# Optimization experiments

Hardware: AMD Instinct MI355X
Metric: run time of the kernel (lower is better)

Reference implementation:

```python
import jax, jax.numpy as jnp
import numpy as np

K_H, K_W = 3, 3
STRIDE, PAD = 1, 1
GN_GROUPS = 32
EPS = 1e-5


def setup_inputs() -> dict:
    key = jax.random.key(0)
    k1, k2, k3 = jax.random.split(key, 3)
    B, C, H, W = 4, 256, 64, 64
    Cout = 256
    x = jax.random.normal(k1, (B, C, H, W), jnp.float32)
    offset = jax.random.normal(k2, (B, 2 * K_H * K_W, H, W), jnp.float32)
    weight = jax.random.normal(k3, (Cout, C, K_H, K_W), jnp.float32) * 0.02
    gamma = jnp.ones((Cout,), jnp.float32)
    beta = jnp.zeros((Cout,), jnp.float32)
    return {"x": x, "offset": offset, "weight": weight, "gamma": gamma, "beta": beta}


def _deform_conv(x, offset, weight):
    B, C, H, W = x.shape
    Cout = weight.shape[0]
    K = K_H * K_W
    Ho = (H + 2 * PAD - K_H) // STRIDE + 1
    Wo = (W + 2 * PAD - K_W) // STRIDE + 1
    ky, kx = jnp.meshgrid(jnp.arange(K_H), jnp.arange(K_W), indexing='ij')
    ky = ky.reshape(K).astype(x.dtype)
    kx = kx.reshape(K).astype(x.dtype)
    # base sampling positions per kernel tap
    py_base = (jnp.arange(Ho) * STRIDE - PAD).astype(x.dtype)[None, :] + ky[:, None]  # [K,Ho]
    px_base = (jnp.arange(Wo) * STRIDE - PAD).astype(x.dtype)[None, :] + kx[:, None]  # [K,Wo]
    off = offset.reshape(B, K, 2, Ho, Wo)  # mmcv layout: (dy, dx) pairs per tap
    py = py_base[None, :, :, None] + off[:, :, 0]  # [B,K,Ho,Wo]
    px = px_base[None, :, None, :] + off[:, :, 1]  # [B,K,Ho,Wo]
    y0 = jnp.floor(py)
    x0 = jnp.floor(px)
    ly = py - y0
    lx = px - x0
    xf = x.reshape(B, C, H * W)

    def gather(yi, xi):
        valid = (yi >= 0) & (yi <= H - 1) & (xi >= 0) & (xi <= W - 1)
        yc = jnp.clip(yi, 0, H - 1).astype(jnp.int32)
        xc = jnp.clip(xi, 0, W - 1).astype(jnp.int32)
        idx = yc * W + xc  # [B,K,Ho,Wo]
        vals = jax.vmap(lambda xb, ib: xb[:, ib])(xf, idx)  # [B,C,K,Ho,Wo]
        return vals * valid[:, None].astype(x.dtype)

    g00 = gather(y0, x0)
    g01 = gather(y0, x0 + 1)
    g10 = gather(y0 + 1, x0)
    g11 = gather(y0 + 1, x0 + 1)
    wy = ly[:, None]  # [B,1,K,Ho,Wo]
    wx = lx[:, None]
    val = ((1 - wy) * (1 - wx) * g00 + (1 - wy) * wx * g01
           + wy * (1 - wx) * g10 + wy * wx * g11)  # [B,C,K,Ho,Wo]
    return jnp.einsum('bckhw,ock->bohw', val, weight.reshape(Cout, C, K))


def reference(x, offset, weight, gamma, beta):
    y = _deform_conv(x, offset, weight)  # [B,Cout,Ho,Wo]
    B, C, H, W = y.shape
    yg = y.reshape(B, GN_GROUPS, C // GN_GROUPS, H, W)
    mean = jnp.mean(yg, axis=(2, 3, 4), keepdims=True)
    var = jnp.var(yg, axis=(2, 3, 4), keepdims=True)
    yn = ((yg - mean) * jax.lax.rsqrt(var + EPS)).reshape(B, C, H, W)
    out = yn * gamma[None, :, None, None] + beta[None, :, None, None]
    return jax.nn.relu(out)
```

## Files before the change

kernel.cpp:

```cpp
#include <hip/hip_runtime.h>

typedef unsigned short ushort_t;
typedef __bf16 bf16x8 __attribute__((ext_vector_type(8)));
typedef float f32x4 __attribute__((ext_vector_type(4)));
typedef void __attribute__((address_space(1))) gvoid_t;
typedef void __attribute__((address_space(3))) lvoid_t;

__device__ __forceinline__ float bflo(unsigned u) { return __builtin_bit_cast(float, u << 16); }
__device__ __forceinline__ float bfhi(unsigned u) { return __builtin_bit_cast(float, u & 0xffff0000u); }
__device__ __forceinline__ unsigned f2bf_bits(float f) {
  unsigned u = __builtin_bit_cast(unsigned, f);
  return (u + 0x7fffu + ((u >> 16) & 1u)) >> 16;
}
__device__ __forceinline__ ushort_t f2bf(float f) { return (ushort_t)f2bf_bits(f); }

#define VMWAIT(N) asm volatile("s_waitcnt vmcnt(" #N ")" ::: "memory")
#define LGKM0 asm volatile("s_waitcnt lgkmcnt(0)" ::: "memory")

__global__ __launch_bounds__(256) void k_prep_w(const float* __restrict__ w,
                                                ushort_t* __restrict__ wb) {
  const int idx = blockIdx.x * 256 + threadIdx.x;
  const float* src = w + (size_t)idx * 9;
  #pragma unroll
  for (int k = 0; k < 9; ++k)
    wb[(k << 16) + idx] = f2bf(src[k]);
}

__global__ __launch_bounds__(256) void k_prep_x(const float* __restrict__ x,
                                                ushort_t* __restrict__ xt) {
  __shared__ ushort_t tile[64][68];
  const int bid = blockIdx.x;
  const int b = bid >> 8;
  const int ct = (bid >> 6) & 3;
  const int pt = bid & 63;
  const int t = threadIdx.x;
  const float* xb = x + ((size_t)(b * 256 + ct * 64)) * 4096 + pt * 64;
  #pragma unroll
  for (int i = 0; i < 16; ++i) {
    const int idx = t + 256 * i;
    const int c_l = idx >> 6, p_l = idx & 63;
    tile[c_l][p_l] = f2bf(xb[(size_t)c_l * 4096 + p_l]);
  }
  __syncthreads();
  ushort_t* xo = xt + ((size_t)(b * 4096 + pt * 64)) * 256 + ct * 64;
  #pragma unroll
  for (int i = 0; i < 16; ++i) {
    const int idx = t + 256 * i;
    const int p_l = idx >> 6, c_l = idx & 63;
    xo[(size_t)p_l * 256 + c_l] = tile[c_l][p_l];
  }
}

struct SMeta {
  float w00, w01, w10, w11;
  int i00, i01, i10, i11;
};
__device__ __forceinline__ SMeta meta_for(int h, int gw, int k, float oy, float ox) {
  SMeta m;
  const float py = (float)(h - 1 + k / 3) + oy;
  const float px = (float)(gw - 1 + k % 3) + ox;
  const float fy = floorf(py), fx = floorf(px);
  const float ly = py - fy, lx = px - fx;
  const int iy0 = (int)fy, ix0 = (int)fx;
  const float vy0 = (iy0 >= 0 && iy0 < 64) ? 1.f : 0.f;
  const float vy1 = (iy0 >= -1 && iy0 < 63) ? 1.f : 0.f;
  const float vx0 = (ix0 >= 0 && ix0 < 64) ? 1.f : 0.f;
  const float vx1 = (ix0 >= -1 && ix0 < 63) ? 1.f : 0.f;
  m.w00 = (1.f - ly) * (1.f - lx) * vy0 * vx0;
  m.w01 = (1.f - ly) * lx * vy0 * vx1;
  m.w10 = ly * (1.f - lx) * vy1 * vx0;
  m.w11 = ly * lx * vy1 * vx1;
  const int cy0 = min(max(iy0, 0), 63), cy1 = min(max(iy0 + 1, 0), 63);
  const int cx0 = min(max(ix0, 0), 63), cx1 = min(max(ix0 + 1, 0), 63);
  m.i00 = (cy0 * 64 + cx0) * 256;
  m.i01 = (cy0 * 64 + cx1) * 256;
  m.i10 = (cy1 * 64 + cx0) * 256;
  m.i11 = (cy1 * 64 + cx1) * 256;
  return m;
}

__device__ __forceinline__ unsigned lerp_pack(unsigned a, unsigned b, unsigned c, unsigned d,
                                              float w00, float w01, float w10, float w11) {
  float lo = w00 * bflo(a) + w01 * bflo(b) + w10 * bflo(c) + w11 * bflo(d);
  float hi = w00 * bfhi(a) + w01 * bfhi(b) + w10 * bfhi(c) + w11 * bfhi(d);
  return f2bf_bits(lo) | (f2bf_bits(hi) << 16);
}

__global__ __launch_bounds__(512) void k_gemm(const float* __restrict__ off,
                                              const ushort_t* __restrict__ xt,
                                              const ushort_t* __restrict__ wb,
                                              float* __restrict__ y,
                                              float* __restrict__ stats) {
  __shared__ __attribute__((aligned(16))) ushort_t Abuf[2][64 * 64];
  __shared__ __attribute__((aligned(16))) ushort_t Bbuf[3][256 * 64];

  const int bid = blockIdx.x;
  const int lb = ((bid & 7) << 5) | (bid >> 3);
  const int b = lb >> 6;
  const int h = lb & 63;
  const int t = threadIdx.x;
  const int wave = t >> 6;
  const int lane = t & 63;
  const int wq = lane >> 4;
  const int wr = lane & 15;
  const int wm = wave >> 2;
  const int wn = wave & 3;

  const int s_w = t >> 3;
  const int c8 = t & 7;

  const f32x4 zero = {0.f, 0.f, 0.f, 0.f};
  f32x4 acc[2][4];
  #pragma unroll
  for (int i = 0; i < 2; ++i)
    #pragma unroll
    for (int j = 0; j < 4; ++j) acc[i][j] = zero;

  const ushort_t* xtb = xt + (size_t)b * 4096 * 256;

  float oy[9], ox[9];
  {
    const float* offb = off + (size_t)b * 18 * 4096 + h * 64 + s_w;
    #pragma unroll
    for (int k = 0; k < 9; ++k) {
      oy[k] = offb[(2 * k) * 4096];
      ox[k] = offb[(2 * k + 1) * 4096];
    }
  }

#define GATHER_ISSUE(TAP, C0)                             \
  {                                                       \
    m = meta_for(h, s_w, (TAP), oy[(TAP)], ox[(TAP)]);    \
    const int cc = (C0) + c8 * 8;                         \
    q00 = *(const uint4*)(xtb + m.i00 + cc);              \
    q01 = *(const uint4*)(xtb + m.i01 + cc);              \
    q10 = *(const uint4*)(xtb + m.i10 + cc);              \
    q11 = *(const uint4*)(xtb + m.i11 + cc);              \
  }

#define B_ISSUE(TAP, C0, BUF)                                                                \
  {                                                                                          \
    _Pragma("unroll") for (int i_ = 0; i_ < 4; ++i_) {                                       \
      const int idx_ = i_ * 512 + t;                                                         \
      const int row_ = idx_ >> 3, slot_ = idx_ & 7;                                          \
      const ushort_t* g_ = wb + ((TAP) << 16) + row_ * 256 + (C0) + ((slot_ ^ (row_ & 7)) << 3); \
      __builtin_amdgcn_global_load_lds((gvoid_t*)g_,                                         \
                                       (lvoid_t*)((char*)&Bbuf[(BUF)][0] + idx_ * 16), 16,   \
                                       0, 0);                                                \
    }                                                                                        \
  }

#define A_WRITE(BUF)                                                         \
  {                                                                          \
    uint4 r;                                                                 \
    r.x = lerp_pack(q00.x, q01.x, q10.x, q11.x, m.w00, m.w01, m.w10, m.w11); \
    r.y = lerp_pack(q00.y, q01.y, q10.y, q11.y, m.w00, m.w01, m.w10, m.w11); \
    r.z = lerp_pack(q00.z, q01.z, q10.z, q11.z, m.w00, m.w01, m.w10, m.w11); \
    r.w = lerp_pack(q00.w, q01.w, q10.w, q11.w, m.w00, m.w01, m.w10, m.w11); \
    *(uint4*)&Abuf[(BUF)][s_w * 64 + ((c8 ^ (s_w & 7)) << 3)] = r;           \
  }

  {
    uint4 q00, q01, q10, q11;
    SMeta m;
    GATHER_ISSUE(0, 0);
    B_ISSUE(0, 0, 0);
    B_ISSUE(0, 64, 1);
    VMWAIT(8);
    A_WRITE(0);
    LGKM0;
    __builtin_amdgcn_s_barrier();
  }

  #pragma unroll
  for (int n = 0; n < 36; ++n) {
    const int curB = n % 3;
    const int curA = n & 1;
    uint4 q00, q01, q10, q11;
    SMeta m;
    if (n < 35) {
      GATHER_ISSUE((n + 1) >> 2, ((n + 1) & 3) << 6);
    }
    if (n < 34) {
      B_ISSUE((n + 2) >> 2, ((n + 2) & 3) << 6, (n + 2) % 3);
    }
    VMWAIT(12);
    #pragma unroll
    for (int ks = 0; ks < 2; ++ks) {
      bf16x8 af[2], bfr[4];
      #pragma unroll
      for (int tm = 0; tm < 2; ++tm) {
        const int row = wm * 32 + tm * 16 + wr;
        const int slot = (ks * 4 + wq) ^ (row & 7);
        af[tm] = *(const bf16x8*)&Abuf[curA][row * 64 + slot * 8];
      }
      #pragma unroll
      for (int tn = 0; tn < 4; ++tn) {
        const int row = wn * 64 + tn * 16 + wr;
        const int slot = (ks * 4 + wq) ^ (row & 7);
        bfr[tn] = *(const bf16x8*)&Bbuf[curB][row * 64 + slot * 8];
      }
      #pragma unroll
      for (int tm = 0; tm < 2; ++tm)
        #pragma unroll
        for (int tn = 0; tn < 4; ++tn)
          acc[tm][tn] =
              __builtin_amdgcn_mfma_f32_16x16x32_bf16(af[tm], bfr[tn], acc[tm][tn], 0, 0, 0);
    }
    if (n < 35) {
      if (n == 34) {
        VMWAIT(0);
      } else {
        VMWAIT(4);
      }
      A_WRITE((n + 1) & 1);
      LGKM0;
      __builtin_amdgcn_s_barrier();
    }
  }
#undef GATHER_ISSUE
#undef B_ISSUE
#undef A_WRITE

  float* yb = y + ((size_t)(b * 4096 + h * 64)) * 256;
  #pragma unroll
  for (int tm = 0; tm < 2; ++tm) {
    #pragma unroll
    for (int tn = 0; tn < 4; ++tn) {
      const int o = wn * 64 + tn * 16 + wr;
      #pragma unroll
      for (int r2 = 0; r2 < 4; ++r2) {
        const int ww = wm * 32 + tm * 16 + wq * 4 + r2;
        yb[ww * 256 + o] = acc[tm][tn][r2];
      }
    }
  }
  #pragma unroll
  for (int tn = 0; tn < 4; ++tn) {
    float sum = 0.f, ss = 0.f;
    #pragma unroll
    for (int tm = 0; tm < 2; ++tm)
      #pragma unroll
      for (int r2 = 0; r2 < 4; ++r2) {
        const float v = acc[tm][tn][r2];
        sum += v;
        ss += v * v;
      }
    sum += __shfl_xor(sum, 16, 64);
    ss += __shfl_xor(ss, 16, 64);
    sum += __shfl_xor(sum, 32, 64);
    ss += __shfl_xor(ss, 32, 64);
    #pragma unroll
    for (int d = 1; d < 8; d <<= 1) {
      sum += __shfl_xor(sum, d, 64);
      ss += __shfl_xor(ss, d, 64);
    }
    if (wq == 0 && (wr & 7) == 0) {
      const int gi = wn * 8 + tn * 2 + (wr >> 3);
      atomicAdd(&stats[(b * 32 + gi) * 2], sum);
      atomicAdd(&stats[(b * 32 + gi) * 2 + 1], ss);
    }
  }
}

__global__ __launch_bounds__(256) void k_apply(const float* __restrict__ y,
                                               const float* __restrict__ stats,
                                               const float* __restrict__ gamma,
                                               const float* __restrict__ beta,
                                               float* __restrict__ out) {
  __shared__ float tile[64][65];
  __shared__ float sm[8], sr[8], sg[64], sb[64];
  const int bid = blockIdx.x;
  const int lb = ((bid & 7) << 7) | (bid >> 3);
  const int b = lb >> 8;
  const int st = (lb >> 2) & 63;
  const int ot = lb & 3;
  const int t = threadIdx.x;
  if (t < 8) {
    const int g = ot * 8 + t;
    const float s1 = stats[(b * 32 + g) * 2];
    const float s2 = stats[(b * 32 + g) * 2 + 1];
    const float mean = s1 * (1.f / 32768.f);
    const float var = s2 * (1.f / 32768.f) - mean * mean;
    sm[t] = mean;
    sr[t] = rsqrtf(var + 1e-5f);
  }
  if (t < 64) {
    sg[t] = gamma[ot * 64 + t];
    sb[t] = beta[ot * 64 + t];
  }
  const float* yb = y + ((size_t)(b * 4096 + st * 64)) * 256 + ot * 64;
  #pragma unroll
  for (int i = 0; i < 16; ++i) {
    const int idx = t + 256 * i;
    const int s_l = idx >> 6, o_l = idx & 63;
    tile[s_l][o_l] = yb[(size_t)s_l * 256 + o_l];
  }
  __syncthreads();
  float* ob = out + ((size_t)(b * 256 + ot * 64)) * 4096 + st * 64;
  #pragma unroll
  for (int i = 0; i < 16; ++i) {
    const int idx = t + 256 * i;
    const int o_l = idx >> 6, s_l = idx & 63;
    const int g = o_l >> 3;
    float v = (tile[s_l][o_l] - sm[g]) * sr[g] * sg[o_l] + sb[o_l];
    v = v > 0.f ? v : 0.f;
    ob[(size_t)o_l * 4096 + s_l] = v;
  }
}

extern "C" void kernel_launch(void* const* d_in, const int* in_sizes, int n_in,
                              void* d_out, int out_size, void* d_ws, size_t ws_size,
                              hipStream_t stream) {
  const float* x = (const float*)d_in[0];
  const float* off = (const float*)d_in[1];
  const float* w = (const float*)d_in[2];
  const float* gamma = (const float*)d_in[3];
  const float* beta = (const float*)d_in[4];
  float* out = (float*)d_out;

  char* ws = (char*)d_ws;
  float* y = (float*)(ws);
  ushort_t* xt = (ushort_t*)(ws + 16777216);
  ushort_t* wb = (ushort_t*)(ws + 25165824);
  float* stats = (float*)(ws + 26345472);

  hipMemsetAsync(stats, 0, 1024, stream);
  k_prep_w<<<256, 256, 0, stream>>>(w, wb);
  k_prep_x<<<1024, 256, 0, stream>>>(x, xt);
  k_gemm<<<256, 512, 0, stream>>>(off, xt, wb, y, stats);
  k_apply<<<1024, 256, 0, stream>>>(y, stats, gamma, beta, out);
}
```

Before: 93.75 us.

## Split GEMM reduction dimension across two blocks and combine partials in bf16

```diff
diff --git a/kernel.cpp b/kernel.cpp
--- a/kernel.cpp
+++ b/kernel.cpp
@@ -8,14 +8,14 @@
 
 __device__ __forceinline__ float bflo(unsigned u) { return __builtin_bit_cast(float, u << 16); }
 __device__ __forceinline__ float bfhi(unsigned u) { return __builtin_bit_cast(float, u & 0xffff0000u); }
+__device__ __forceinline__ float bf2f(ushort_t v) {
+  return __builtin_bit_cast(float, ((unsigned)v) << 16);
+}
 __device__ __forceinline__ unsigned f2bf_bits(float f) {
   unsigned u = __builtin_bit_cast(unsigned, f);
   return (u + 0x7fffu + ((u >> 16) & 1u)) >> 16;
 }
 __device__ __forceinline__ ushort_t f2bf(float f) { return (ushort_t)f2bf_bits(f); }
-
-#define VMWAIT(N) asm volatile("s_waitcnt vmcnt(" #N ")" ::: "memory")
-#define LGKM0 asm volatile("s_waitcnt lgkmcnt(0)" ::: "memory")
 
 __global__ __launch_bounds__(256) void k_prep_w(const float* __restrict__ w,
                                                 ushort_t* __restrict__ wb) {
@@ -86,16 +86,122 @@
   return f2bf_bits(lo) | (f2bf_bits(hi) << 16);
 }
 
+template <int KH>
+__device__ __forceinline__ void run_gemm(const float* __restrict__ offb,
+                                         const ushort_t* __restrict__ xtb,
+                                         const ushort_t* __restrict__ wb,
+                                         ushort_t* Ab, ushort_t* Bb,
+                                         int h, int s_w, int c8, int t,
+                                         int wm, int wn, int wq, int wr,
+                                         f32x4 (&acc)[2][4]) {
+  float oy[5], ox[5];
+  #pragma unroll
+  for (int i = 0; i < 5; ++i) {
+    oy[i] = offb[(2 * (KH * 4 + i)) * 4096];
+    ox[i] = offb[(2 * (KH * 4 + i) + 1) * 4096];
+  }
+
+#define GATHER(N)                                                \
+  {                                                              \
+    const int c_ = KH * 18 + (N);                                \
+    const int tap_ = c_ >> 2;                                    \
+    const int loc_ = tap_ - KH * 4;                              \
+    const int c0_ = (c_ & 3) << 6;                               \
+    m = meta_for(h, s_w, tap_, oy[loc_], ox[loc_]);              \
+    const int cc_ = c0_ + c8 * 8;                                \
+    q00 = *(const uint4*)(xtb + m.i00 + cc_);                    \
+    q01 = *(const uint4*)(xtb + m.i01 + cc_);                    \
+    q10 = *(const uint4*)(xtb + m.i10 + cc_);                    \
+    q11 = *(const uint4*)(xtb + m.i11 + cc_);                    \
+  }
+
+#define B_ISSUE(N, BUF)                                                                        \
+  {                                                                                            \
+    const int c_ = KH * 18 + (N);                                                              \
+    const int tap_ = c_ >> 2;                                                                  \
+    const int c0_ = (c_ & 3) << 6;                                                             \
+    _Pragma("unroll") for (int i_ = 0; i_ < 4; ++i_) {                                         \
+      const int idx_ = i_ * 512 + t;                                                           \
+      const int row_ = idx_ >> 3, slot_ = idx_ & 7;                                            \
+      const ushort_t* g_ = wb + (tap_ << 16) + row_ * 256 + c0_ + ((slot_ ^ (row_ & 7)) << 3); \
+      __builtin_amdgcn_global_load_lds(                                                        \
+          (gvoid_t*)g_, (lvoid_t*)((char*)Bb + (BUF) * 32768 + idx_ * 16), 16, 0, 0);          \
+    }                                                                                          \
+  }
+
+#define A_WRITE(BUF)                                                         \
+  {                                                                          \
+    uint4 r;                                                                 \
+    r.x = lerp_pack(q00.x, q01.x, q10.x, q11.x, m.w00, m.w01, m.w10, m.w11); \
+    r.y = lerp_pack(q00.y, q01.y, q10.y, q11.y, m.w00, m.w01, m.w10, m.w11); \
+    r.z = lerp_pack(q00.z, q01.z, q10.z, q11.z, m.w00, m.w01, m.w10, m.w11); \
+    r.w = lerp_pack(q00.w, q01.w, q10.w, q11.w, m.w00, m.w01, m.w10, m.w11); \
+    *(uint4*)&Ab[(BUF) * 4096 + s_w * 64 + ((c8 ^ (s_w & 7)) << 3)] = r;     \
+  }
+
+  {
+    SMeta m;
+    uint4 q00, q01, q10, q11;
+    B_ISSUE(0, 0);
+    GATHER(0);
+    A_WRITE(0);
+  }
+  __syncthreads();
+
+  #pragma unroll
+  for (int n = 0; n < 18; ++n) {
+    const int cur = n & 1;
+    const int nb = cur ^ 1;
+    SMeta m;
+    uint4 q00, q01, q10, q11;
+    if (n < 17) {
+      B_ISSUE(n + 1, nb);
+      GATHER(n + 1);
+    }
+    #pragma unroll
+    for (int ks = 0; ks < 2; ++ks) {
+      bf16x8 af[2], bfr[4];
+      #pragma unroll
+      for (int tm = 0; tm < 2; ++tm) {
+        const int row = wm * 32 + tm * 16 + wr;
+        const int slot = (ks * 4 + wq) ^ (row & 7);
+        af[tm] = *(const bf16x8*)&Ab[cur * 4096 + row * 64 + slot * 8];
+      }
+      #pragma unroll
+      for (int tn = 0; tn < 4; ++tn) {
+        const int row = wn * 64 + tn * 16 + wr;
+        const int slot = (ks * 4 + wq) ^ (row & 7);
+        bfr[tn] = *(const bf16x8*)&Bb[cur * 16384 + row * 64 + slot * 8];
+      }
+      #pragma unroll
+      for (int tm = 0; tm < 2; ++tm)
+        #pragma unroll
+        for (int tn = 0; tn < 4; ++tn)
+          acc[tm][tn] =
+              __builtin_amdgcn_mfma_f32_16x16x32_bf16(af[tm], bfr[tn], acc[tm][tn], 0, 0, 0);
+    }
+    if (n < 17) {
+      A_WRITE(nb);
+      __syncthreads();
+    }
+  }
+#undef GATHER
+#undef B_ISSUE
+#undef A_WRITE
+}
+
 __global__ __launch_bounds__(512) void k_gemm(const float* __restrict__ off,
                                               const ushort_t* __restrict__ xt,
                                               const ushort_t* __restrict__ wb,
-                                              float* __restrict__ y,
-                                              float* __restrict__ stats) {
+                                              ushort_t* __restrict__ y0,
+                                              ushort_t* __restrict__ y1) {
   __shared__ __attribute__((aligned(16))) ushort_t Abuf[2][64 * 64];
-  __shared__ __attribute__((aligned(16))) ushort_t Bbuf[3][256 * 64];
+  __shared__ __attribute__((aligned(16))) ushort_t Bbuf[2][256 * 64];
 
   const int bid = blockIdx.x;
-  const int lb = ((bid & 7) << 5) | (bid >> 3);
+  const int rowid = bid & 255;
+  const int kh = bid >> 8;
+  const int lb = ((rowid & 7) << 5) | (rowid >> 3);
   const int b = lb >> 6;
   const int h = lb & 63;
   const int t = threadIdx.x;
@@ -105,7 +211,6 @@
   const int wr = lane & 15;
   const int wm = wave >> 2;
   const int wn = wave & 3;
-
   const int s_w = t >> 3;
   const int c8 = t & 7;
 
@@ -117,112 +222,14 @@
     for (int j = 0; j < 4; ++j) acc[i][j] = zero;
 
   const ushort_t* xtb = xt + (size_t)b * 4096 * 256;
-
-  float oy[9], ox[9];
-  {
-    const float* offb = off + (size_t)b * 18 * 4096 + h * 64 + s_w;
-    #pragma unroll
-    for (int k = 0; k < 9; ++k) {
-      oy[k] = offb[(2 * k) * 4096];
-      ox[k] = offb[(2 * k + 1) * 4096];
-    }
-  }
-
-#define GATHER_ISSUE(TAP, C0)                             \
-  {                                                       \
-    m = meta_for(h, s_w, (TAP), oy[(TAP)], ox[(TAP)]);    \
-    const int cc = (C0) + c8 * 8;                         \
-    q00 = *(const uint4*)(xtb + m.i00 + cc);              \
-    q01 = *(const uint4*)(xtb + m.i01 + cc);              \
-    q10 = *(const uint4*)(xtb + m.i10 + cc);              \
-    q11 = *(const uint4*)(xtb + m.i11 + cc);              \
-  }
-
-#define B_ISSUE(TAP, C0, BUF)                                                                \
-  {                                                                                          \
-    _Pragma("unroll") for (int i_ = 0; i_ < 4; ++i_) {                                       \
-      const int idx_ = i_ * 512 + t;                                                         \
-      const int row_ = idx_ >> 3, slot_ = idx_ & 7;                                          \
-      const ushort_t* g_ = wb + ((TAP) << 16) + row_ * 256 + (C0) + ((slot_ ^ (row_ & 7)) << 3); \
-      __builtin_amdgcn_global_load_lds((gvoid_t*)g_,                                         \
-                                       (lvoid_t*)((char*)&Bbuf[(BUF)][0] + idx_ * 16), 16,   \
-                                       0, 0);                                                \
-    }                                                                                        \
-  }
-
-#define A_WRITE(BUF)                                                         \
-  {                                                                          \
-    uint4 r;                                                                 \
-    r.x = lerp_pack(q00.x, q01.x, q10.x, q11.x, m.w00, m.w01, m.w10, m.w11); \
-    r.y = lerp_pack(q00.y, q01.y, q10.y, q11.y, m.w00, m.w01, m.w10, m.w11); \
-    r.z = lerp_pack(q00.z, q01.z, q10.z, q11.z, m.w00, m.w01, m.w10, m.w11); \
-    r.w = lerp_pack(q00.w, q01.w, q10.w, q11.w, m.w00, m.w01, m.w10, m.w11); \
-    *(uint4*)&Abuf[(BUF)][s_w * 64 + ((c8 ^ (s_w & 7)) << 3)] = r;           \
-  }
-
-  {
-    uint4 q00, q01, q10, q11;
-    SMeta m;
-    GATHER_ISSUE(0, 0);
-    B_ISSUE(0, 0, 0);
-    B_ISSUE(0, 64, 1);
-    VMWAIT(8);
-    A_WRITE(0);
-    LGKM0;
-    __builtin_amdgcn_s_barrier();
-  }
-
-  #pragma unroll
-  for (int n = 0; n < 36; ++n) {
-    const int curB = n % 3;
-    const int curA = n & 1;
-    uint4 q00, q01, q10, q11;
-    SMeta m;
-    if (n < 35) {
-      GATHER_ISSUE((n + 1) >> 2, ((n + 1) & 3) << 6);
-    }
-    if (n < 34) {
-      B_ISSUE((n + 2) >> 2, ((n + 2) & 3) << 6, (n + 2) % 3);
-    }
-    VMWAIT(12);
-    #pragma unroll
-    for (int ks = 0; ks < 2; ++ks) {
-      bf16x8 af[2], bfr[4];
-      #pragma unroll
-      for (int tm = 0; tm < 2; ++tm) {
-        const int row = wm * 32 + tm * 16 + wr;
-        const int slot = (ks * 4 + wq) ^ (row & 7);
-        af[tm] = *(const bf16x8*)&Abuf[curA][row * 64 + slot * 8];
-      }
-      #pragma unroll
-      for (int tn = 0; tn < 4; ++tn) {
-        const int row = wn * 64 + tn * 16 + wr;
-        const int slot = (ks * 4 + wq) ^ (row & 7);
-        bfr[tn] = *(const bf16x8*)&Bbuf[curB][row * 64 + slot * 8];
-      }
-      #pragma unroll
-      for (int tm = 0; tm < 2; ++tm)
-        #pragma unroll
-        for (int tn = 0; tn < 4; ++tn)
-          acc[tm][tn] =
-              __builtin_amdgcn_mfma_f32_16x16x32_bf16(af[tm], bfr[tn], acc[tm][tn], 0, 0, 0);
-    }
-    if (n < 35) {
-      if (n == 34) {
-        VMWAIT(0);
-      } else {
-        VMWAIT(4);
-      }
-      A_WRITE((n + 1) & 1);
-      LGKM0;
-      __builtin_amdgcn_s_barrier();
-    }
-  }
-#undef GATHER_ISSUE
-#undef B_ISSUE
-#undef A_WRITE
-
-  float* yb = y + ((size_t)(b * 4096 + h * 64)) * 256;
+  const float* offb = off + (size_t)b * 18 * 4096 + h * 64 + s_w;
+
+  if (kh == 0)
+    run_gemm<0>(offb, xtb, wb, &Abuf[0][0], &Bbuf[0][0], h, s_w, c8, t, wm, wn, wq, wr, acc);
+  else
+    run_gemm<1>(offb, xtb, wb, &Abuf[0][0], &Bbuf[0][0], h, s_w, c8, t, wm, wn, wq, wr, acc);
+
+  ushort_t* yb = (kh ? y1 : y0) + ((size_t)(b * 4096 + h * 64)) * 256;
   #pragma unroll
   for (int tm = 0; tm < 2; ++tm) {
     #pragma unroll
@@ -231,39 +238,62 @@
       #pragma unroll
       for (int r2 = 0; r2 < 4; ++r2) {
         const int ww = wm * 32 + tm * 16 + wq * 4 + r2;
-        yb[ww * 256 + o] = acc[tm][tn][r2];
+        yb[ww * 256 + o] = f2bf(acc[tm][tn][r2]);
       }
     }
   }
-  #pragma unroll
-  for (int tn = 0; tn < 4; ++tn) {
-    float sum = 0.f, ss = 0.f;
-    #pragma unroll
-    for (int tm = 0; tm < 2; ++tm)
-      #pragma unroll
-      for (int r2 = 0; r2 < 4; ++r2) {
-        const float v = acc[tm][tn][r2];
-        sum += v;
-        ss += v * v;
-      }
-    sum += __shfl_xor(sum, 16, 64);
-    ss += __shfl_xor(ss, 16, 64);
-    sum += __shfl_xor(sum, 32, 64);
-    ss += __shfl_xor(ss, 32, 64);
-    #pragma unroll
-    for (int d = 1; d < 8; d <<= 1) {
-      sum += __shfl_xor(sum, d, 64);
-      ss += __shfl_xor(ss, d, 64);
-    }
-    if (wq == 0 && (wr & 7) == 0) {
-      const int gi = wn * 8 + tn * 2 + (wr >> 3);
-      atomicAdd(&stats[(b * 32 + gi) * 2], sum);
-      atomicAdd(&stats[(b * 32 + gi) * 2 + 1], ss);
-    }
-  }
-}
-
-__global__ __launch_bounds__(256) void k_apply(const float* __restrict__ y,
+}
+
+__global__ __launch_bounds__(256) void k_comb(const ushort_t* __restrict__ y0,
+                                              const ushort_t* __restrict__ y1,
+                                              ushort_t* __restrict__ yc,
+                                              float* __restrict__ stats) {
+  const int bid = blockIdx.x;
+  const int lb = ((bid & 7) << 5) | (bid >> 3);
+  const int b = lb >> 6;
+  const int sc = lb & 63;
+  const int t = threadIdx.x;
+  const int og = t & 31;
+  const int s0 = t >> 5;
+  const size_t base = ((size_t)(b * 4096 + sc * 64)) * 256 + og * 8;
+  float sum = 0.f, ss = 0.f;
+  #pragma unroll
+  for (int i = 0; i < 8; ++i) {
+    const size_t o8 = base + (size_t)(s0 + i * 8) * 256;
+    const uint4 a = *(const uint4*)(y0 + o8);
+    const uint4 c = *(const uint4*)(y1 + o8);
+    uint4 r;
+    {
+      float vl = bflo(a.x) + bflo(c.x), vh = bfhi(a.x) + bfhi(c.x);
+      r.x = f2bf_bits(vl) | (f2bf_bits(vh) << 16);
+      sum += vl + vh; ss += vl * vl + vh * vh;
+    }
+    {
+      float vl = bflo(a.y) + bflo(c.y), vh = bfhi(a.y) + bfhi(c.y);
+      r.y = f2bf_bits(vl) | (f2bf_bits(vh) << 16);
+      sum += vl + vh; ss += vl * vl + vh * vh;
+    }
+    {
+      float vl = bflo(a.z) + bflo(c.z), vh = bfhi(a.z) + bfhi(c.z);
+      r.z = f2bf_bits(vl) | (f2bf_bits(vh) << 16);
+      sum += vl + vh; ss += vl * vl + vh * vh;
+    }
+    {
+      float vl = bflo(a.w) + bflo(c.w), vh = bfhi(a.w) + bfhi(c.w);
+      r.w = f2bf_bits(vl) | (f2bf_bits(vh) << 16);
+      sum += vl + vh; ss += vl * vl + vh * vh;
+    }
+    *(uint4*)(yc + o8) = r;
+  }
+  sum += __shfl_xor(sum, 32, 64);
+  ss += __shfl_xor(ss, 32, 64);
+  if ((t & 63) < 32) {
+    atomicAdd(&stats[(b * 32 + og) * 2], sum);
+    atomicAdd(&stats[(b * 32 + og) * 2 + 1], ss);
+  }
+}
+
+__global__ __launch_bounds__(256) void k_apply(const ushort_t* __restrict__ yc,
                                                const float* __restrict__ stats,
                                                const float* __restrict__ gamma,
                                                const float* __restrict__ beta,
@@ -289,12 +319,12 @@
     sg[t] = gamma[ot * 64 + t];
     sb[t] = beta[ot * 64 + t];
   }
-  const float* yb = y + ((size_t)(b * 4096 + st * 64)) * 256 + ot * 64;
+  const ushort_t* yb = yc + ((size_t)(b * 4096 + st * 64)) * 256 + ot * 64;
   #pragma unroll
   for (int i = 0; i < 16; ++i) {
     const int idx = t + 256 * i;
     const int s_l = idx >> 6, o_l = idx & 63;
-    tile[s_l][o_l] = yb[(size_t)s_l * 256 + o_l];
+    tile[s_l][o_l] = bf2f(yb[(size_t)s_l * 256 + o_l]);
   }
   __syncthreads();
   float* ob = out + ((size_t)(b * 256 + ot * 64)) * 4096 + st * 64;
@@ -320,14 +350,17 @@
   float* out = (float*)d_out;
 
   char* ws = (char*)d_ws;
-  float* y = (float*)(ws);
+  ushort_t* y0 = (ushort_t*)(ws);
+  ushort_t* y1 = (ushort_t*)(ws + 8388608);
   ushort_t* xt = (ushort_t*)(ws + 16777216);
+  ushort_t* yc = xt;
   ushort_t* wb = (ushort_t*)(ws + 25165824);
   float* stats = (float*)(ws + 26345472);
 
   hipMemsetAsync(stats, 0, 1024, stream);
   k_prep_w<<<256, 256, 0, stream>>>(w, wb);
   k_prep_x<<<1024, 256, 0, stream>>>(x, xt);
-  k_gemm<<<256, 512, 0, stream>>>(off, xt, wb, y, stats);
-  k_apply<<<1024, 256, 0, stream>>>(y, stats, gamma, beta, out);
-}
+  k_gemm<<<512, 512, 0, stream>>>(off, xt, wb, y0, y1);
+  k_comb<<<256, 256, 0, stream>>>(y0, y1, yc, stats);
+  k_apply<<<1024, 256, 0, stream>>>(yc, stats, gamma, beta, out);
+}
```

New measurement: 87.46 us. -6.7%, faster.
